# Optimization experiments

Measured on AMD Instinct MI355X. Metric: run time of the kernel, lower is better.

The kernel has to match this reference:

```python
import jax, jax.numpy as jnp
import numpy as np

B, T, D = 2, 2048, 1024
NH, NKV, HD = 16, 4, 64
ROPE = 16  # partial RoPE dims (first 16 of 64)
HALF = ROPE // 2


def apply_rope(x, cos, sin):
    # x: (B, nH, T, HD); rotate first ROPE dims, pass the rest through
    x1 = x[..., :HALF]
    x2 = x[..., HALF:ROPE]
    xp = x[..., ROPE:]
    c = cos[None, None, :, :]  # (1,1,T,HALF)
    s = sin[None, None, :, :]
    return jnp.concatenate([x1 * c - x2 * s, x1 * s + x2 * c, xp], axis=-1)


def setup_inputs() -> dict:
    key = jax.random.key(0)
    k0, k1, k2 = jax.random.split(key, 3)
    x = jax.random.normal(k0, (B, T, D), dtype=jnp.float32)
    # RoPE tables for the rotated sub-dimension (half = ROPE//2 = 8)
    inv_freq = 1.0 / (10000.0 ** (jnp.arange(HALF, dtype=jnp.float32) / HALF))
    ang = jnp.arange(T, dtype=jnp.float32)[:, None] * inv_freq[None, :]
    cos = jnp.cos(ang)
    sin = jnp.sin(ang)
    attn_mask = jnp.tril(jnp.ones((T, T), dtype=bool))  # causal
    w_qkv = jax.random.normal(k1, ((NH + 2 * NKV) * HD, D), dtype=jnp.float32) * (D ** -0.5)
    w_out = jax.random.normal(k2, (D, D), dtype=jnp.float32) * (D ** -0.5)
    q_scale = jnp.full((NH, 1), 1.5, dtype=jnp.float32)
    k_scale = jnp.full((NKV, 1), 1.5, dtype=jnp.float32)
    return {"x": x, "cos": cos, "sin": sin, "attn_mask": attn_mask,
            "w_qkv": w_qkv, "w_out": w_out, "q_scale": q_scale, "k_scale": k_scale}


def reference(x, cos, sin, attn_mask, w_qkv, w_out, q_scale, k_scale):
    Bx, Tx, C = x.shape
    groups = NH // NKV
    qkv = x @ w_qkv.T  # (B,T,(NH+2*NKV)*HD)
    q, k, v = jnp.split(qkv, [NH * HD, (NH + NKV) * HD], axis=-1)
    q = q.reshape(Bx, Tx, NH, HD).transpose(0, 2, 1, 3)    # (B,NH,T,HD)
    k = k.reshape(Bx, Tx, NKV, HD).transpose(0, 2, 1, 3)   # (B,NKV,T,HD)
    v = v.reshape(Bx, Tx, NKV, HD).transpose(0, 2, 1, 3)
    # per-head qk gain scaling
    q = q * q_scale[None, :, :, None]  # (1,NH,1,1)
    k = k * k_scale[None, :, :, None]
    # partial RoPE on q and k
    q = apply_rope(q, cos[:Tx], sin[:Tx])
    k = apply_rope(k, cos[:Tx], sin[:Tx])
    # GQA expand (repeat_interleave along heads)
    ke = jnp.repeat(k, groups, axis=1)  # (B,NH,T,HD)
    ve = jnp.repeat(v, groups, axis=1)
    # scaled dot-product attention with causal mask
    scores = jnp.einsum('bhqd,bhkd->bhqk', q, ke) * (HD ** -0.5)
    scores = jnp.where(attn_mask[None, None], scores, -jnp.inf)
    probs = jax.nn.softmax(scores, axis=-1)
    ao = jnp.einsum('bhqk,bhkd->bhqd', probs, ve)  # (B,NH,T,HD)
    # xsa: subtract self-component along the (shared) kv value direction
    ao_r = ao.reshape(Bx, NKV, groups, Tx, HD)
    vv = v[:, :, None]  # (B,NKV,1,T,HD), broadcasts over groups
    dots = jnp.sum(ao_r * vv, axis=-1, keepdims=True)
    norm = jnp.maximum(jnp.sum(vv * vv, axis=-1, keepdims=True), 1e-8)
    ao = (ao_r - (dots / norm) * vv).reshape(Bx, NH, Tx, HD)
    out = ao.transpose(0, 2, 1, 3).reshape(Bx, Tx, C) @ w_out.T
    return out
```

## Files before the change

### kernel.cpp

```cpp
#include <hip/hip_runtime.h>
#include <hip/hip_bf16.h>

#define NB 2
#define NT 2048
#define ND 1024
#define NHEADS 16
#define NKVH 4
#define HDIM 64
#define QKVD 1536

typedef __attribute__((ext_vector_type(8))) short short8;
typedef __attribute__((ext_vector_type(4))) float floatx4;

#if defined(__has_builtin)
#  if __has_builtin(__builtin_amdgcn_global_load_lds)
#    define HAS_GLL 1
#  endif
#endif
#ifndef HAS_GLL
#  define HAS_GLL 0
#endif

__device__ __forceinline__ void gll16(const void* g, void* l, int lane) {
#if HAS_GLL
  (void)lane;
  __builtin_amdgcn_global_load_lds(
      (const __attribute__((address_space(1))) unsigned int*)g,
      (__attribute__((address_space(3))) unsigned int*)l, 16, 0, 0);
#else
  *(short8*)((short*)l) = *(const short8*)g;
#endif
}

__device__ __forceinline__ unsigned short f2bf(float f) {
  union { float f; unsigned int u; } cv; cv.f = f;
  unsigned int u = cv.u;
  u += 0x7fffu + ((u >> 16) & 1u);
  return (unsigned short)(u >> 16);
}
__device__ __forceinline__ float bf2f(unsigned short u) {
  union { unsigned int u; float f; } cv; cv.u = ((unsigned int)u) << 16; return cv.f;
}

#define N4_X   1048576
#define N4_WQ   393216
#define N4_WO   262144
__global__ __launch_bounds__(256) void cvt_all(
    const float* __restrict__ x, const float* __restrict__ wq,
    const float* __restrict__ wo,
    unsigned short* __restrict__ xb, unsigned short* __restrict__ wqb,
    unsigned short* __restrict__ wob) {
  int i = blockIdx.x * 256 + threadIdx.x;
  const float* src; unsigned short* dst; int j;
  if (i < N4_X)              { src = x;  dst = xb;  j = i; }
  else if (i < N4_X + N4_WQ) { src = wq; dst = wqb; j = i - N4_X; }
  else                       { src = wo; dst = wob; j = i - N4_X - N4_WQ; }
  float4 v = ((const float4*)src)[j];
  ushort4 o;
  o.x = f2bf(v.x); o.y = f2bf(v.y); o.z = f2bf(v.z); o.w = f2bf(v.w);
  ((ushort4*)dst)[j] = o;
}


#define GEMM1W_PROLOGUE(Aptr, Bptr, Kdim)                                      \
  __shared__ __align__(16) short As[2][64][32];                                \
  __shared__ __align__(16) short Bs[2][64][32];                                \
  const int lane = threadIdx.x;                                                \
  const int quad = lane >> 4, l16 = lane & 15;                                 \
  const int srow = lane >> 2;                                                  \
  const int sch  = ((lane & 3) ^ (srow & 3)) * 8;                              \
  const unsigned short* agp = (Aptr) + (size_t)(m0 + srow) * (Kdim) + sch;     \
  const unsigned short* bgp = (Bptr) + (size_t)(n0 + srow) * (Kdim) + sch;     \
  short* asb = &As[0][0][0];                                                   \
  short* bsb = &Bs[0][0][0];                                                   \
  const int lofs = (HAS_GLL ? 0 : lane * 8);                                   \
  const int cs = (quad ^ (l16 & 3)) * 8;                                       \
  floatx4 acc[4][4] = {};                                                      \
  _Pragma("unroll")                                                            \
  for (int g = 0; g < 4; g++) {                                                \
    gll16(agp + (size_t)(16 * g) * (Kdim), asb + g * 512 + lofs, lane);        \
    gll16(bgp + (size_t)(16 * g) * (Kdim), bsb + g * 512 + lofs, lane);        \
  }                                                                            \
  const int NIT = (Kdim) / 32;                                                 \
  for (int it = 0; it < NIT; it++) {                                           \
    __syncthreads();                                                           \
    const int bi = it & 1, bn = bi ^ 1;                                        \
    if (it + 1 < NIT) {                                                        \
      const int k = (it + 1) * 32;                                             \
      _Pragma("unroll")                                                        \
      for (int g = 0; g < 4; g++) {                                            \
        gll16(agp + (size_t)(16 * g) * (Kdim) + k, asb + bn * 2048 + g * 512 + lofs, lane); \
        gll16(bgp + (size_t)(16 * g) * (Kdim) + k, bsb + bn * 2048 + g * 512 + lofs, lane); \
      }                                                                        \
    }                                                                          \
    short8 af[4], bf[4];                                                       \
    _Pragma("unroll")                                                          \
    for (int mi = 0; mi < 4; mi++) af[mi] = *(const short8*)&As[bi][mi * 16 + l16][cs]; \
    _Pragma("unroll")                                                          \
    for (int ni = 0; ni < 4; ni++) bf[ni] = *(const short8*)&Bs[bi][ni * 16 + l16][cs]; \
    _Pragma("unroll")                                                          \
    for (int mi = 0; mi < 4; mi++)                                             \
      _Pragma("unroll")                                                        \
      for (int ni = 0; ni < 4; ni++)                                           \
        acc[mi][ni] = __builtin_amdgcn_mfma_f32_16x16x32_bf16(af[mi], bf[ni], acc[mi][ni], 0, 0, 0); \
  }

__global__ __launch_bounds__(64) void gemm_qkv(
    const unsigned short* __restrict__ A,
    const unsigned short* __restrict__ Bm,
    const float* __restrict__ cosT, const float* __restrict__ sinT,
    const float* __restrict__ q_scale, const float* __restrict__ k_scale,
    unsigned short* __restrict__ qb, unsigned short* __restrict__ kb,
    unsigned short* __restrict__ vtb)
{
  const int m0 = blockIdx.x * 64, n0 = blockIdx.y * 64;
  GEMM1W_PROLOGUE(A, Bm, ND)

  const int hh = blockIdx.y;
  const int lo8 = l16 & 7;

  if (hh >= NHEADS + NKVH) {
    const int kvh = hh - (NHEADS + NKVH);
#pragma unroll
    for (int mi = 0; mi < 4; mi++) {
      const int mrow = m0 + mi * 16 + quad * 4;
      const int bb = mrow >> 11, tt = mrow & (NT - 1);
#pragma unroll
      for (int ni = 0; ni < 4; ni++) {
        const int d = ni * 16 + l16;
        ushort4 w;
        w.x = f2bf(acc[mi][ni][0]); w.y = f2bf(acc[mi][ni][1]);
        w.z = f2bf(acc[mi][ni][2]); w.w = f2bf(acc[mi][ni][3]);
        *(ushort4*)(vtb + ((size_t)((bb * NKVH + kvh) * HDIM + d)) * NT + tt) = w;
      }
    }
  } else {
    float scl; unsigned short* dst0; int hloc, nh;
    if (hh < NHEADS) { scl = q_scale[hh] * (0.125f * 1.44269504088896f); hloc = hh; dst0 = qb; nh = NHEADS; }
    else             { scl = k_scale[hh - NHEADS]; hloc = hh - NHEADS; dst0 = kb; nh = NKVH; }
#pragma unroll
    for (int mi = 0; mi < 4; mi++) {
#pragma unroll
      for (int r = 0; r < 4; r++) {
        const int mrow = m0 + mi * 16 + quad * 4 + r;
        const int bb = mrow >> 11, tt = mrow & (NT - 1);
        unsigned short* drow = dst0 + ((size_t)((bb * nh + hloc) * NT + tt)) * HDIM;

        const float own = acc[mi][0][r];
        const float oth = __shfl_xor(own, 8);
        const float c = cosT[tt * 8 + lo8], s = sinT[tt * 8 + lo8];
        const float roped = (l16 < 8) ? (own * c - oth * s)
                                      : (oth * s + own * c);
        drow[l16] = f2bf(roped * scl);
#pragma unroll
        for (int ni = 1; ni < 4; ni++)
          drow[ni * 16 + l16] = f2bf(acc[mi][ni][r] * scl);
      }
    }
  }
}

__global__ __launch_bounds__(64) void gemm_out(
    const unsigned short* __restrict__ A,
    const unsigned short* __restrict__ Bm,
    float* __restrict__ C, int M, int N, int K)
{
  const int m0 = blockIdx.x * 64, n0 = blockIdx.y * 64;
  GEMM1W_PROLOGUE(A, Bm, K)

#pragma unroll
  for (int mi = 0; mi < 4; mi++)
#pragma unroll
    for (int ni = 0; ni < 4; ni++)
#pragma unroll
      for (int r = 0; r < 4; r++) {
        int m = m0 + mi * 16 + quad * 4 + r;
        int n = n0 + ni * 16 + l16;
        C[(size_t)m * N + n] = acc[mi][ni][r];
      }
}

__global__ __launch_bounds__(256) void fattn(
    const unsigned short* __restrict__ qb,
    const unsigned short* __restrict__ kb,
    const unsigned short* __restrict__ vtb,
    unsigned short* __restrict__ aob,
    float* __restrict__ pbuf)
{
  const int idx = blockIdx.x;
  const int h = blockIdx.y, b = blockIdx.z;
  const int kv = h >> 2;

  int qt, j0, cnt, chunk; bool direct;
  if (idx < 16) { qt = 16 + idx; j0 = 0; cnt = 16; chunk = 0; direct = false; }
  else {
    int rel = idx - 16, s = 16 - (rel >> 1);
    if ((rel & 1) == 0) { qt = s - 1;  j0 = 0;  cnt = s; chunk = 0; direct = true;  }
    else                { qt = s + 15; j0 = 16; cnt = s; chunk = 1; direct = false; }
  }

  const int tid = threadIdx.x;
  const int wid = tid >> 6, lane = tid & 63;
  const int quad = lane >> 4, l16 = lane & 15;
  const int hi8 = l16 >> 3, lo8 = l16 & 7;

  __shared__ __align__(16) short Ks[2][64][64];
  __shared__ __align__(16) short Vs[2][64][64];
  __shared__ __align__(16) short Ps[4][16][64];

  const unsigned short* qg = qb + ((size_t)((b * NHEADS + h) * NT + qt * 64)) * HDIM;
  const int qrow = wid * 16 + l16;
  short8 aq0 = *(const short8*)(qg + (size_t)qrow * HDIM + quad * 8);
  short8 aq1 = *(const short8*)(qg + (size_t)qrow * HDIM + 32 + quad * 8);

  const int sr  = tid >> 3;
  const int lck = ((tid & 7) ^ (sr & 7)) * 8;
  const unsigned short* kgp0 = kb  + ((size_t)((b * NKVH + kv) * NT) + sr) * HDIM + lck;
  const unsigned short* vgp0 = vtb + ((size_t)((b * NKVH + kv) * HDIM) + sr) * NT + lck;
  short* ksb = &Ks[0][0][0];
  short* vsb = &Vs[0][0][0];
  const int lofs = (HAS_GLL ? wid * 512 : tid * 8);

  const int cs0 = (quad ^ lo8) * 8;
  const int cs1 = cs0 ^ 32;

  int pwo[4][4];
#pragma unroll
  for (int r = 0; r < 4; r++) {
    const int row = quad * 4 + r;
#pragma unroll
    for (int nb = 0; nb < 4; nb++)
      pwo[r][nb] = wid * 1024 + row * 64 + (((nb * 2 + hi8) ^ (row & 7)) * 8) + lo8;
  }
  short* psf = &Ps[0][0][0];

  floatx4 acc_o[4] = {};
  float lsum[4] = {0.f, 0.f, 0.f, 0.f};

  {
    const unsigned short* kg = kgp0 + (size_t)j0 * 64 * HDIM;
    const unsigned short* vg = vgp0 + j0 * 64;
    gll16(kg, ksb + lofs, lane);
    gll16(kg + 32 * HDIM, ksb + 2048 + lofs, lane);
    gll16(vg, vsb + lofs, lane);
    gll16(vg + (size_t)32 * NT, vsb + 2048 + lofs, lane);
  }

  for (int i = 0; i < cnt; i++) {
    const int jt = j0 + i;
    __syncthreads();
    const int bi = i & 1, bn = bi ^ 1;
    if (i + 1 < cnt) {
      const unsigned short* kg = kgp0 + (size_t)(jt + 1) * 64 * HDIM;
      const unsigned short* vg = vgp0 + (jt + 1) * 64;
      gll16(kg, ksb + bn * 4096 + lofs, lane);
      gll16(kg + 32 * HDIM, ksb + bn * 4096 + 2048 + lofs, lane);
      gll16(vg, vsb + bn * 4096 + lofs, lane);
      gll16(vg + (size_t)32 * NT, vsb + bn * 4096 + 2048 + lofs, lane);
    }

    floatx4 s[4] = {};
#pragma unroll
    for (int nb = 0; nb < 4; nb++) {
      short8 bk0 = *(const short8*)&Ks[bi][nb * 16 + l16][cs0];
      short8 bk1 = *(const short8*)&Ks[bi][nb * 16 + l16][cs1];
      s[nb] = __builtin_amdgcn_mfma_f32_16x16x32_bf16(aq0, bk0, s[nb], 0, 0, 0);
      s[nb] = __builtin_amdgcn_mfma_f32_16x16x32_bf16(aq1, bk1, s[nb], 0, 0, 0);
    }

    if (jt == qt) {
#pragma unroll
      for (int nb = 0; nb < 4; nb++) {
        int col = nb * 16 + l16;
#pragma unroll
        for (int r = 0; r < 4; r++)
          if (col > wid * 16 + quad * 4 + r) s[nb][r] = -INFINITY;
      }
    }

#pragma unroll
    for (int r = 0; r < 4; r++) {
#pragma unroll
      for (int nb = 0; nb < 4; nb++) {
        float p = __builtin_amdgcn_exp2f(s[nb][r]);
        lsum[r] += p;
        psf[pwo[r][nb]] = (short)(__float_as_uint(p) >> 16);
      }
    }

    short8 ap0 = *(const short8*)&Ps[wid][l16][cs0];
    short8 ap1 = *(const short8*)&Ps[wid][l16][cs1];
#pragma unroll
    for (int nb = 0; nb < 4; nb++) {
      short8 bv0 = *(const short8*)&Vs[bi][nb * 16 + l16][cs0];
      short8 bv1 = *(const short8*)&Vs[bi][nb * 16 + l16][cs1];
      acc_o[nb] = __builtin_amdgcn_mfma_f32_16x16x32_bf16(ap0, bv0, acc_o[nb], 0, 0, 0);
      acc_o[nb] = __builtin_amdgcn_mfma_f32_16x16x32_bf16(ap1, bv1, acc_o[nb], 0, 0, 0);
    }
  }

  const int bl = (cnt - 1) & 1;

  if (direct) {
#pragma unroll
    for (int r = 0; r < 4; r++) {
      float ls = lsum[r];
#pragma unroll
      for (int off = 1; off < 16; off <<= 1) ls += __shfl_xor(ls, off);
      const float invl = 1.f / ls;

      const int rowl = wid * 16 + quad * 4 + r;
      const int vcol = ((rowl >> 3) ^ lo8) * 8 + (rowl & 7);
      float vd[4], dot = 0.f, vv = 0.f;
#pragma unroll
      for (int nb = 0; nb < 4; nb++) {
        vd[nb] = bf2f((unsigned short)Vs[bl][nb * 16 + l16][vcol]);
        dot += acc_o[nb][r] * invl * vd[nb];
        vv  += vd[nb] * vd[nb];
      }
#pragma unroll
      for (int off = 1; off < 16; off <<= 1) {
        dot += __shfl_xor(dot, off);
        vv  += __shfl_xor(vv, off);
      }
      const float coef = dot / fmaxf(vv, 1e-8f);
      unsigned short* dst = aob + ((size_t)(b * NT + qt * 64 + rowl)) * ND + h * HDIM + l16;
#pragma unroll
      for (int nb = 0; nb < 4; nb++)
        dst[nb * 16] = f2bf(acc_o[nb][r] * invl - coef * vd[nb]);
    }
  } else {
    const int slot = ((b * NHEADS + h) * 16 + (qt - 16)) * 2 + chunk;
    float* pO = pbuf + (size_t)slot * 4160;
    float* pl = pO + 4096;
#pragma unroll
    for (int r = 0; r < 4; r++) {
      float ls = lsum[r];
#pragma unroll
      for (int off = 1; off < 16; off <<= 1) ls += __shfl_xor(ls, off);
      const int rowl = wid * 16 + quad * 4 + r;
      if (l16 == 0) pl[rowl] = ls;
#pragma unroll
      for (int nb = 0; nb < 4; nb++)
        pO[rowl * 64 + nb * 16 + l16] = acc_o[nb][r];
    }
  }
}

__global__ __launch_bounds__(256) void redn(
    const float* __restrict__ pbuf,
    const unsigned short* __restrict__ vtb,
    unsigned short* __restrict__ aob)
{
  const int qt = 16 + blockIdx.x;
  const int h = blockIdx.y, b = blockIdx.z;
  const int kv = h >> 2;
  const int tid = threadIdx.x;

  const int slot0 = ((b * NHEADS + h) * 16 + blockIdx.x) * 2;
  const float* O0 = pbuf + (size_t)slot0 * 4160;
  const float* O1 = O0 + 4160;
  const float* l0 = O0 + 4096;
  const float* l1 = O1 + 4096;

  __shared__ short vt[64][66];

  {
    const int d = tid >> 2, tq = (tid & 3) * 16;
    const unsigned short* src = vtb + ((size_t)((b * NKVH + kv) * HDIM + d)) * NT + qt * 64 + tq;
    short8 v0 = *(const short8*)src;
    short8 v1 = *(const short8*)(src + 8);
    *(short8*)&vt[d][tq] = v0;
    *(short8*)&vt[d][tq + 8] = v1;
  }
  __syncthreads();

  const int row = tid >> 2, dq = tid & 3;
  const float invl = 1.f / (l0[row] + l1[row]);

  float o[16], vd[16];
  float dot = 0.f, vv = 0.f;
#pragma unroll
  for (int j = 0; j < 16; j++) {
    const int d = dq * 16 + j;
    float ov = (O0[row * 64 + d] + O1[row * 64 + d]) * invl;
    float v  = bf2f((unsigned short)vt[d][row]);
    o[j] = ov; vd[j] = v;
    dot += ov * v; vv += v * v;
  }
  dot += __shfl_xor(dot, 1); dot += __shfl_xor(dot, 2);
  vv  += __shfl_xor(vv, 1);  vv  += __shfl_xor(vv, 2);
  const float coef = dot / fmaxf(vv, 1e-8f);

  unsigned short* dst = aob + ((size_t)(b * NT + qt * 64 + row)) * ND + h * HDIM + dq * 16;
  ushort4 w0, w1, w2, w3;
  w0.x = f2bf(o[0] - coef * vd[0]);  w0.y = f2bf(o[1] - coef * vd[1]);
  w0.z = f2bf(o[2] - coef * vd[2]);  w0.w = f2bf(o[3] - coef * vd[3]);
  w1.x = f2bf(o[4] - coef * vd[4]);  w1.y = f2bf(o[5] - coef * vd[5]);
  w1.z = f2bf(o[6] - coef * vd[6]);  w1.w = f2bf(o[7] - coef * vd[7]);
  w2.x = f2bf(o[8] - coef * vd[8]);  w2.y = f2bf(o[9] - coef * vd[9]);
  w2.z = f2bf(o[10] - coef * vd[10]); w2.w = f2bf(o[11] - coef * vd[11]);
  w3.x = f2bf(o[12] - coef * vd[12]); w3.y = f2bf(o[13] - coef * vd[13]);
  w3.z = f2bf(o[14] - coef * vd[14]); w3.w = f2bf(o[15] - coef * vd[15]);
  ((ushort4*)dst)[0] = w0; ((ushort4*)dst)[1] = w1;
  ((ushort4*)dst)[2] = w2; ((ushort4*)dst)[3] = w3;
}

extern "C" void kernel_launch(void* const* d_in, const int* in_sizes, int n_in,
                              void* d_out, int out_size, void* d_ws, size_t ws_size,
                              hipStream_t stream) {
  const float* x       = (const float*)d_in[0];
  const float* cosT    = (const float*)d_in[1];
  const float* sinT    = (const float*)d_in[2];
  const float* w_qkv   = (const float*)d_in[4];
  const float* w_out   = (const float*)d_in[5];
  const float* q_scale = (const float*)d_in[6];
  const float* k_scale = (const float*)d_in[7];
  float* out = (float*)d_out;

  char* ws = (char*)d_ws;
  unsigned short* xb    = (unsigned short*)ws;
  unsigned short* wqkvb = (unsigned short*)(ws + 8388608);
  float*          pbuf  = (float*)ws;
  unsigned short* woutb = (unsigned short*)(ws + 17825792);
  unsigned short* qb    = (unsigned short*)(ws + 19922944);
  unsigned short* kb    = (unsigned short*)(ws + 28311552);
  unsigned short* vtb   = (unsigned short*)(ws + 30408704);
  unsigned short* aob   = (unsigned short*)(ws + 32505856);

  cvt_all<<<(N4_X + N4_WQ + N4_WO) / 256, 256, 0, stream>>>(
      x, w_qkv, w_out, xb, wqkvb, woutb);

  gemm_qkv<<<dim3(NB * NT / 64, QKVD / 64), 64, 0, stream>>>(
      xb, wqkvb, cosT, sinT, q_scale, k_scale, qb, kb, vtb);

  fattn<<<dim3(48, NHEADS, NB), 256, 0, stream>>>(qb, kb, vtb, aob, pbuf);
  redn<<<dim3(16, NHEADS, NB), 256, 0, stream>>>(pbuf, vtb, aob);

  gemm_out<<<dim3(NB * NT / 64, ND / 64), 64, 0, stream>>>(
      aob, woutb, out, NB * NT, ND, ND);
}
```

Measured before the change: 193.5 us.

## Load MFMA operands directly from global memory instead of LDS staging

Drops the double-buffered LDS staging (global_load_lds plus barriers) in both GEMMs and the attention kernel, and loads MFMA fragments straight from global memory into registers, relying on the caches for reuse. The GEMMs also switch to a 1D grid with an 8x8 swizzled tile order so neighbouring blocks share row tiles in L2. This removes barriers and LDS traffic, but each lane now issues strided 16-byte global loads with no explicit prefetch, and the K/V tiles are re-read by every wave of the attention block rather than shared through LDS.

After: 353.9 us. 83.0% more time.

```diff
diff --git a/kernel.cpp b/kernel.cpp
--- a/kernel.cpp
+++ b/kernel.cpp
@@ -11,26 +11,6 @@
 
 typedef __attribute__((ext_vector_type(8))) short short8;
 typedef __attribute__((ext_vector_type(4))) float floatx4;
-
-#if defined(__has_builtin)
-#  if __has_builtin(__builtin_amdgcn_global_load_lds)
-#    define HAS_GLL 1
-#  endif
-#endif
-#ifndef HAS_GLL
-#  define HAS_GLL 0
-#endif
-
-__device__ __forceinline__ void gll16(const void* g, void* l, int lane) {
-#if HAS_GLL
-  (void)lane;
-  __builtin_amdgcn_global_load_lds(
-      (const __attribute__((address_space(1))) unsigned int*)g,
-      (__attribute__((address_space(3))) unsigned int*)l, 16, 0, 0);
-#else
-  *(short8*)((short*)l) = *(const short8*)g;
-#endif
-}
 
 __device__ __forceinline__ unsigned short f2bf(float f) {
   union { float f; unsigned int u; } cv; cv.f = f;
@@ -62,49 +42,6 @@
 }
 
 
-#define GEMM1W_PROLOGUE(Aptr, Bptr, Kdim)                                      \
-  __shared__ __align__(16) short As[2][64][32];                                \
-  __shared__ __align__(16) short Bs[2][64][32];                                \
-  const int lane = threadIdx.x;                                                \
-  const int quad = lane >> 4, l16 = lane & 15;                                 \
-  const int srow = lane >> 2;                                                  \
-  const int sch  = ((lane & 3) ^ (srow & 3)) * 8;                              \
-  const unsigned short* agp = (Aptr) + (size_t)(m0 + srow) * (Kdim) + sch;     \
-  const unsigned short* bgp = (Bptr) + (size_t)(n0 + srow) * (Kdim) + sch;     \
-  short* asb = &As[0][0][0];                                                   \
-  short* bsb = &Bs[0][0][0];                                                   \
-  const int lofs = (HAS_GLL ? 0 : lane * 8);                                   \
-  const int cs = (quad ^ (l16 & 3)) * 8;                                       \
-  floatx4 acc[4][4] = {};                                                      \
-  _Pragma("unroll")                                                            \
-  for (int g = 0; g < 4; g++) {                                                \
-    gll16(agp + (size_t)(16 * g) * (Kdim), asb + g * 512 + lofs, lane);        \
-    gll16(bgp + (size_t)(16 * g) * (Kdim), bsb + g * 512 + lofs, lane);        \
-  }                                                                            \
-  const int NIT = (Kdim) / 32;                                                 \
-  for (int it = 0; it < NIT; it++) {                                           \
-    __syncthreads();                                                           \
-    const int bi = it & 1, bn = bi ^ 1;                                        \
-    if (it + 1 < NIT) {                                                        \
-      const int k = (it + 1) * 32;                                             \
-      _Pragma("unroll")                                                        \
-      for (int g = 0; g < 4; g++) {                                            \
-        gll16(agp + (size_t)(16 * g) * (Kdim) + k, asb + bn * 2048 + g * 512 + lofs, lane); \
-        gll16(bgp + (size_t)(16 * g) * (Kdim) + k, bsb + bn * 2048 + g * 512 + lofs, lane); \
-      }                                                                        \
-    }                                                                          \
-    short8 af[4], bf[4];                                                       \
-    _Pragma("unroll")                                                          \
-    for (int mi = 0; mi < 4; mi++) af[mi] = *(const short8*)&As[bi][mi * 16 + l16][cs]; \
-    _Pragma("unroll")                                                          \
-    for (int ni = 0; ni < 4; ni++) bf[ni] = *(const short8*)&Bs[bi][ni * 16 + l16][cs]; \
-    _Pragma("unroll")                                                          \
-    for (int mi = 0; mi < 4; mi++)                                             \
-      _Pragma("unroll")                                                        \
-      for (int ni = 0; ni < 4; ni++)                                           \
-        acc[mi][ni] = __builtin_amdgcn_mfma_f32_16x16x32_bf16(af[mi], bf[ni], acc[mi][ni], 0, 0, 0); \
-  }
-
 __global__ __launch_bounds__(64) void gemm_qkv(
     const unsigned short* __restrict__ A,
     const unsigned short* __restrict__ Bm,
@@ -113,11 +50,33 @@
     unsigned short* __restrict__ qb, unsigned short* __restrict__ kb,
     unsigned short* __restrict__ vtb)
 {
-  const int m0 = blockIdx.x * 64, n0 = blockIdx.y * 64;
-  GEMM1W_PROLOGUE(A, Bm, ND)
-
-  const int hh = blockIdx.y;
+  const int bid = blockIdx.x;
+  const int mt = (bid & 7) * 8 + ((bid >> 3) & 7);
+  const int hh = bid >> 6;
+  const int m0 = mt * 64, n0 = hh * 64;
+  const int K = ND;
+
+  const int lane = threadIdx.x;
+  const int quad = lane >> 4, l16 = lane & 15;
   const int lo8 = l16 & 7;
+
+  const unsigned short* ar = A  + (size_t)(m0 + l16) * K + quad * 8;
+  const unsigned short* br = Bm + (size_t)(n0 + l16) * K + quad * 8;
+
+  floatx4 acc[4][4] = {};
+#pragma unroll 2
+  for (int k0 = 0; k0 < K; k0 += 32) {
+    short8 af[4], bf[4];
+#pragma unroll
+    for (int mi = 0; mi < 4; mi++) af[mi] = *(const short8*)(ar + (size_t)(mi * 16) * K + k0);
+#pragma unroll
+    for (int ni = 0; ni < 4; ni++) bf[ni] = *(const short8*)(br + (size_t)(ni * 16) * K + k0);
+#pragma unroll
+    for (int mi = 0; mi < 4; mi++)
+#pragma unroll
+      for (int ni = 0; ni < 4; ni++)
+        acc[mi][ni] = __builtin_amdgcn_mfma_f32_16x16x32_bf16(af[mi], bf[ni], acc[mi][ni], 0, 0, 0);
+  }
 
   if (hh >= NHEADS + NKVH) {
     const int kvh = hh - (NHEADS + NKVH);
@@ -165,8 +124,31 @@
     const unsigned short* __restrict__ Bm,
     float* __restrict__ C, int M, int N, int K)
 {
-  const int m0 = blockIdx.x * 64, n0 = blockIdx.y * 64;
-  GEMM1W_PROLOGUE(A, Bm, K)
+  const int bid = blockIdx.x;
+  const int mt = (bid & 7) * 8 + ((bid >> 3) & 7);
+  const int nt = bid >> 6;
+  const int m0 = mt * 64, n0 = nt * 64;
+
+  const int lane = threadIdx.x;
+  const int quad = lane >> 4, l16 = lane & 15;
+
+  const unsigned short* ar = A  + (size_t)(m0 + l16) * K + quad * 8;
+  const unsigned short* br = Bm + (size_t)(n0 + l16) * K + quad * 8;
+
+  floatx4 acc[4][4] = {};
+#pragma unroll 2
+  for (int k0 = 0; k0 < K; k0 += 32) {
+    short8 af[4], bf[4];
+#pragma unroll
+    for (int mi = 0; mi < 4; mi++) af[mi] = *(const short8*)(ar + (size_t)(mi * 16) * K + k0);
+#pragma unroll
+    for (int ni = 0; ni < 4; ni++) bf[ni] = *(const short8*)(br + (size_t)(ni * 16) * K + k0);
+#pragma unroll
+    for (int mi = 0; mi < 4; mi++)
+#pragma unroll
+      for (int ni = 0; ni < 4; ni++)
+        acc[mi][ni] = __builtin_amdgcn_mfma_f32_16x16x32_bf16(af[mi], bf[ni], acc[mi][ni], 0, 0, 0);
+  }
 
 #pragma unroll
   for (int mi = 0; mi < 4; mi++)
@@ -204,8 +186,6 @@
   const int quad = lane >> 4, l16 = lane & 15;
   const int hi8 = l16 >> 3, lo8 = l16 & 7;
 
-  __shared__ __align__(16) short Ks[2][64][64];
-  __shared__ __align__(16) short Vs[2][64][64];
   __shared__ __align__(16) short Ps[4][16][64];
 
   const unsigned short* qg = qb + ((size_t)((b * NHEADS + h) * NT + qt * 64)) * HDIM;
@@ -213,17 +193,11 @@
   short8 aq0 = *(const short8*)(qg + (size_t)qrow * HDIM + quad * 8);
   short8 aq1 = *(const short8*)(qg + (size_t)qrow * HDIM + 32 + quad * 8);
 
-  const int sr  = tid >> 3;
-  const int lck = ((tid & 7) ^ (sr & 7)) * 8;
-  const unsigned short* kgp0 = kb  + ((size_t)((b * NKVH + kv) * NT) + sr) * HDIM + lck;
-  const unsigned short* vgp0 = vtb + ((size_t)((b * NKVH + kv) * HDIM) + sr) * NT + lck;
-  short* ksb = &Ks[0][0][0];
-  short* vsb = &Vs[0][0][0];
-  const int lofs = (HAS_GLL ? wid * 512 : tid * 8);
+  const unsigned short* krow = kb + ((size_t)((b * NKVH + kv) * NT) + l16) * HDIM + quad * 8;
+  const unsigned short* vrow = vtb + ((size_t)((b * NKVH + kv) * HDIM) + l16) * NT + quad * 8;
 
   const int cs0 = (quad ^ lo8) * 8;
   const int cs1 = cs0 ^ 32;
-
   int pwo[4][4];
 #pragma unroll
   for (int r = 0; r < 4; r++) {
@@ -237,33 +211,16 @@
   floatx4 acc_o[4] = {};
   float lsum[4] = {0.f, 0.f, 0.f, 0.f};
 
-  {
-    const unsigned short* kg = kgp0 + (size_t)j0 * 64 * HDIM;
-    const unsigned short* vg = vgp0 + j0 * 64;
-    gll16(kg, ksb + lofs, lane);
-    gll16(kg + 32 * HDIM, ksb + 2048 + lofs, lane);
-    gll16(vg, vsb + lofs, lane);
-    gll16(vg + (size_t)32 * NT, vsb + 2048 + lofs, lane);
-  }
-
   for (int i = 0; i < cnt; i++) {
     const int jt = j0 + i;
-    __syncthreads();
-    const int bi = i & 1, bn = bi ^ 1;
-    if (i + 1 < cnt) {
-      const unsigned short* kg = kgp0 + (size_t)(jt + 1) * 64 * HDIM;
-      const unsigned short* vg = vgp0 + (jt + 1) * 64;
-      gll16(kg, ksb + bn * 4096 + lofs, lane);
-      gll16(kg + 32 * HDIM, ksb + bn * 4096 + 2048 + lofs, lane);
-      gll16(vg, vsb + bn * 4096 + lofs, lane);
-      gll16(vg + (size_t)32 * NT, vsb + bn * 4096 + 2048 + lofs, lane);
-    }
+    const unsigned short* kf = krow + (size_t)jt * 64 * HDIM;
+    const unsigned short* vf = vrow + jt * 64;
 
     floatx4 s[4] = {};
 #pragma unroll
     for (int nb = 0; nb < 4; nb++) {
-      short8 bk0 = *(const short8*)&Ks[bi][nb * 16 + l16][cs0];
-      short8 bk1 = *(const short8*)&Ks[bi][nb * 16 + l16][cs1];
+      short8 bk0 = *(const short8*)(kf + (size_t)(nb * 16) * HDIM);
+      short8 bk1 = *(const short8*)(kf + (size_t)(nb * 16) * HDIM + 32);
       s[nb] = __builtin_amdgcn_mfma_f32_16x16x32_bf16(aq0, bk0, s[nb], 0, 0, 0);
       s[nb] = __builtin_amdgcn_mfma_f32_16x16x32_bf16(aq1, bk1, s[nb], 0, 0, 0);
     }
@@ -292,15 +249,13 @@
     short8 ap1 = *(const short8*)&Ps[wid][l16][cs1];
 #pragma unroll
     for (int nb = 0; nb < 4; nb++) {
-      short8 bv0 = *(const short8*)&Vs[bi][nb * 16 + l16][cs0];
-      short8 bv1 = *(const short8*)&Vs[bi][nb * 16 + l16][cs1];
+      short8 bv0 = *(const short8*)(vf + (size_t)(nb * 16) * NT);
+      short8 bv1 = *(const short8*)(vf + (size_t)(nb * 16) * NT + 32);
       acc_o[nb] = __builtin_amdgcn_mfma_f32_16x16x32_bf16(ap0, bv0, acc_o[nb], 0, 0, 0);
       acc_o[nb] = __builtin_amdgcn_mfma_f32_16x16x32_bf16(ap1, bv1, acc_o[nb], 0, 0, 0);
     }
   }
 
-  const int bl = (cnt - 1) & 1;
-
   if (direct) {
 #pragma unroll
     for (int r = 0; r < 4; r++) {
@@ -310,11 +265,11 @@
       const float invl = 1.f / ls;
 
       const int rowl = wid * 16 + quad * 4 + r;
-      const int vcol = ((rowl >> 3) ^ lo8) * 8 + (rowl & 7);
+      const unsigned short* vd_p = vtb + ((size_t)((b * NKVH + kv) * HDIM) + l16) * NT + qt * 64 + rowl;
       float vd[4], dot = 0.f, vv = 0.f;
 #pragma unroll
       for (int nb = 0; nb < 4; nb++) {
-        vd[nb] = bf2f((unsigned short)Vs[bl][nb * 16 + l16][vcol]);
+        vd[nb] = bf2f(vd_p[(size_t)(nb * 16) * NT]);
         dot += acc_o[nb][r] * invl * vd[nb];
         vv  += vd[nb] * vd[nb];
       }
@@ -431,12 +386,12 @@
   cvt_all<<<(N4_X + N4_WQ + N4_WO) / 256, 256, 0, stream>>>(
       x, w_qkv, w_out, xb, wqkvb, woutb);
 
-  gemm_qkv<<<dim3(NB * NT / 64, QKVD / 64), 64, 0, stream>>>(
+  gemm_qkv<<<1536, 64, 0, stream>>>(
       xb, wqkvb, cosT, sinT, q_scale, k_scale, qb, kb, vtb);
 
   fattn<<<dim3(48, NHEADS, NB), 256, 0, stream>>>(qb, kb, vtb, aob, pbuf);
   redn<<<dim3(16, NHEADS, NB), 256, 0, stream>>>(pbuf, vtb, aob);
 
-  gemm_out<<<dim3(NB * NT / 64, ND / 64), 64, 0, stream>>>(
+  gemm_out<<<1024, 64, 0, stream>>>(
       aob, woutb, out, NB * NT, ND, ND);
 }
```
